# Optimization experiments

Measured on AMD Instinct MI355X. Metric: run time of the kernel, lower is better.

Reference implementation:

```python
import jax, jax.numpy as jnp
import numpy as np

B, S, H = 2, 2048, 2048
FFN = 1024
E = 8
TOP_K = 2


def setup_inputs() -> dict:
    key = jax.random.key(0)
    ks = jax.random.split(key, 5)
    scale = 0.02
    hidden_states = jax.random.normal(ks[0], (B, S, H), dtype=jnp.float32)
    Wg = jax.random.normal(ks[1], (E, H), dtype=jnp.float32) * scale   # gate: Linear(H, E) weight
    W1 = jax.random.normal(ks[2], (E, FFN, H), dtype=jnp.float32) * scale  # stacked w1 per expert
    W3 = jax.random.normal(ks[3], (E, FFN, H), dtype=jnp.float32) * scale  # stacked w3 per expert
    W2 = jax.random.normal(ks[4], (E, H, FFN), dtype=jnp.float32) * scale  # stacked w2 per expert
    bias = jnp.zeros((E,), dtype=jnp.float32)  # e_score_correction_bias buffer
    return {"hidden_states": hidden_states, "Wg": Wg, "W1": W1, "W2": W2, "W3": W3, "bias": bias}


def reference(hidden_states, Wg, W1, W2, W3, bias):
    bsz, seq_len, hidden_dim = hidden_states.shape
    x = hidden_states.reshape(-1, hidden_dim)                 # [T, H]
    router_logits = x @ Wg.T                                  # [T, E]
    routing_weights = jax.nn.sigmoid(router_logits.astype(jnp.float32))
    scores = routing_weights + bias                           # bias only affects selection
    _, top_k_index = jax.lax.top_k(scores, TOP_K)             # [T, K]
    top_k_weights = jnp.take_along_axis(routing_weights, top_k_index, axis=1)
    top_k_weights = top_k_weights / top_k_weights.sum(axis=-1, keepdims=True)
    top_k_weights = top_k_weights.astype(x.dtype)
    # per-token per-expert combine weight (0 for non-selected experts)
    one_hot = jax.nn.one_hot(top_k_index, Wg.shape[0], dtype=x.dtype)  # [T, K, E]
    expert_w = jnp.einsum('tk,tke->te', top_k_weights, one_hot)        # [T, E]
    # SwiGLU expert MLPs applied via stacked (grouped) GEMMs
    h1 = jnp.einsum('th,efh->tef', x, W1)                     # [T, E, FFN]
    h3 = jnp.einsum('th,efh->tef', x, W3)
    g = jax.nn.silu(h1) * h3 * expert_w[:, :, None]           # scale before down-proj
    out = jnp.einsum('tef,ehf->th', g, W2)                    # weighted combine
    return out.reshape(bsz, seq_len, hidden_dim)
```

## Files before the change

### kernel.cpp

```cpp
#include <hip/hip_runtime.h>
#include <hip/hip_bf16.h>


#define T_TOK 4096
#define H_DIM 2048
#define FFN_D 1024
#define NE    8

typedef __attribute__((ext_vector_type(8))) short          bf16x8;
typedef __attribute__((ext_vector_type(4))) float          f32x4;
typedef __attribute__((ext_vector_type(4))) unsigned short us4;

#define N4_PER_W ((size_t)NE * FFN_D * H_DIM / 4)
#define RB_ROUTER 1024u
#define CB_CONV   8192u

__device__ __forceinline__ unsigned short f2bf(float f) {
  unsigned u = __builtin_bit_cast(unsigned, f);
  u += 0x7fffu + ((u >> 16) & 1u);
  return (unsigned short)(u >> 16);
}
__device__ __forceinline__ float bf2f(unsigned short u) {
  return __builtin_bit_cast(float, ((unsigned)u) << 16);
}
__device__ __forceinline__ void async16(const void* g, void* l) {
  __builtin_amdgcn_global_load_lds((const __attribute__((address_space(1))) void*)g,
                                   (__attribute__((address_space(3))) void*)l, 16, 0, 0);
}

__global__ void router_conv_kernel(const float* __restrict__ x,
                                   const float* __restrict__ Wg,
                                   const float* __restrict__ bias,
                                   unsigned* __restrict__ epair,
                                   float* __restrict__ wpair,
                                   unsigned short* __restrict__ Xb,
                                   const float* __restrict__ W1, unsigned short* __restrict__ W1b,
                                   const float* __restrict__ W3, unsigned short* __restrict__ W3b) {
  if (blockIdx.x >= RB_ROUTER) {
    size_t b0 = (size_t)(blockIdx.x - RB_ROUTER) * 1024;
#pragma unroll
    for (int k = 0; k < 4; k++) {
      size_t i = b0 + k * 256 + threadIdx.x;
      const float* s; unsigned short* d;
      if (i < N4_PER_W) { s = W1; d = W1b; } else { s = W3; d = W3b; i -= N4_PER_W; }
      float4 v = ((const float4*)s)[i];
      us4 o; o.x = f2bf(v.x); o.y = f2bf(v.y); o.z = f2bf(v.z); o.w = f2bf(v.w);
      ((us4*)d)[i] = o;
    }
    return;
  }
  const int wv   = threadIdx.x >> 6;
  const int lane = threadIdx.x & 63;
  const int t    = blockIdx.x * 4 + wv;

  const float4* xr = (const float4*)(x + (size_t)t * H_DIM);
  us4*          xb = (us4*)(Xb + (size_t)t * H_DIM);

  float acc[NE];
#pragma unroll
  for (int e = 0; e < NE; e++) acc[e] = 0.f;

#pragma unroll
  for (int j = 0; j < 8; j++) {
    int i4 = j * 64 + lane;
    float4 v = xr[i4];
    us4 d; d.x = f2bf(v.x); d.y = f2bf(v.y); d.z = f2bf(v.z); d.w = f2bf(v.w);
    xb[i4] = d;
#pragma unroll
    for (int e = 0; e < NE; e++) {
      float4 w = ((const float4*)(Wg + e * H_DIM))[i4];
      acc[e] += v.x * w.x + v.y * w.y + v.z * w.z + v.w * w.w;
    }
  }
#pragma unroll
  for (int e = 0; e < NE; e++) {
#pragma unroll
    for (int m = 32; m >= 1; m >>= 1) acc[e] += __shfl_xor(acc[e], m, 64);
  }

  if (lane == 0) {
    float sig[NE], sc[NE];
#pragma unroll
    for (int e = 0; e < NE; e++) {
      sig[e] = 1.f / (1.f + expf(-acc[e]));
      sc[e]  = sig[e] + bias[e];
    }
    int i1 = 0; float v1 = sc[0];
#pragma unroll
    for (int e = 1; e < NE; e++) if (sc[e] > v1) { v1 = sc[e]; i1 = e; }
    int i2 = -1; float v2 = -1e30f;
#pragma unroll
    for (int e = 0; e < NE; e++) if (e != i1 && sc[e] > v2) { v2 = sc[e]; i2 = e; }
    float w1 = sig[i1], w2 = sig[i2];
    float s = w1 + w2;
    epair[t] = (unsigned)i1 | ((unsigned)i2 << 8);
    wpair[2 * t]     = w1 / s;
    wpair[2 * t + 1] = w2 / s;
  }
}

__global__ void compact_kernel(const unsigned* __restrict__ epair,
                               const float* __restrict__ wpair,
                               int* __restrict__ cnt,
                               int* __restrict__ base,
                               int* __restrict__ rows,
                               float* __restrict__ wts,
                               int* __restrict__ t2s) {
  const int e    = threadIdx.x >> 6;
  const int lane = threadIdx.x & 63;
  const unsigned long long ltmask = ((unsigned long long)1 << lane) - 1;
  __shared__ int cnts[NE];

  int count = 0;
  for (int c = 0; c < T_TOK; c += 64) {
    int t = c + lane;
    unsigned ep = epair[t];
    bool m1 = ((ep & 255u) == (unsigned)e);
    bool m2 = (((ep >> 8) & 255u) == (unsigned)e);
    unsigned long long b1 = __ballot(m1);
    if (m1) {
      int p = count + __popcll(b1 & ltmask);
      rows[e * T_TOK + p] = t;
      wts [e * T_TOK + p] = wpair[2 * t];
      t2s[2 * t] = (e << 12) | p;
    }
    count += __popcll(b1);
    unsigned long long b2 = __ballot(m2);
    if (m2) {
      int p = count + __popcll(b2 & ltmask);
      rows[e * T_TOK + p] = t;
      wts [e * T_TOK + p] = wpair[2 * t + 1];
      t2s[2 * t + 1] = (e << 12) | p;
    }
    count += __popcll(b2);
  }
  if (lane == 0) { cnts[e] = count; cnt[e] = count; }
  __syncthreads();
  if (threadIdx.x == 0) {
    int s = 0;
    for (int i = 0; i < NE; i++) { base[i] = s; s += cnts[i]; }
    base[NE] = s;
  }
}

__launch_bounds__(256)
__global__ void upproj_fast(const unsigned short* __restrict__ Xb,
                            const unsigned short* __restrict__ W1b,
                            const unsigned short* __restrict__ W3b,
                            const int* __restrict__ cnt,
                            const int* __restrict__ base,
                            const int* __restrict__ rows,
                            const float* __restrict__ wts,
                            unsigned short* __restrict__ G,
                            const float* __restrict__ W2, unsigned short* __restrict__ W2b) {
  if (blockIdx.z == NE) {
    size_t flat = (size_t)blockIdx.y * 16 + blockIdx.x;
    size_t b0 = flat * 8192;
#pragma unroll
    for (int k = 0; k < 32; k++) {
      size_t i = b0 + (size_t)k * 256 + threadIdx.x;
      float4 v = ((const float4*)W2)[i];
      us4 o; o.x = f2bf(v.x); o.y = f2bf(v.y); o.z = f2bf(v.z); o.w = f2bf(v.w);
      ((us4*)W2b)[i] = o;
    }
    return;
  }
  const int e  = blockIdx.z;
  const int m0 = blockIdx.y * 128;
  const int n0 = blockIdx.x * 64;
  const int ce = cnt[e];
  if (m0 >= ce) return;

  __shared__ __align__(16) unsigned short As [128 * 32];
  __shared__ __align__(16) unsigned short B1s[64 * 32];
  __shared__ __align__(16) unsigned short B3s[64 * 32];
  __shared__ int   t_ids[128];
  __shared__ float w_lds[128];

  const int tid = threadIdx.x;
  if (tid < 128) {
    int i = m0 + tid;
    if (i < ce) { t_ids[tid] = rows[e * T_TOK + i]; w_lds[tid] = wts[e * T_TOK + i]; }
    else        { t_ids[tid] = 0;                   w_lds[tid] = 0.f; }
  }
  __syncthreads();

  const int lane = tid & 63;
  const int wv   = tid >> 6;

  const unsigned short* gA[2];
#pragma unroll
  for (int c = 0; c < 2; c++) {
    int r = wv * 32 + c * 16 + (lane >> 2);
    gA[c] = Xb + (size_t)t_ids[r] * H_DIM + (lane & 3) * 8;
  }
  const size_t wrow = (size_t)(n0 + wv * 16 + (lane >> 2));
  const unsigned short* gB1 = W1b + (size_t)e * FFN_D * H_DIM + wrow * H_DIM + (lane & 3) * 8;
  const unsigned short* gB3 = W3b + (size_t)e * FFN_D * H_DIM + wrow * H_DIM + (lane & 3) * 8;
  unsigned short* lA0 = &As [(wv * 32 + 0)  * 32];
  unsigned short* lA1 = &As [(wv * 32 + 16) * 32];
  unsigned short* lB1 = &B1s[(wv * 16) * 32];
  unsigned short* lB3 = &B3s[(wv * 16) * 32];

  const int wm = (wv & 1) * 64;
  const int wn = (wv >> 1) * 32;
  const int qk = (lane >> 4) * 8;
  const int lr = lane & 15;

  f32x4 acc1[4][2], acc3[4][2];
#pragma unroll
  for (int mi = 0; mi < 4; mi++)
#pragma unroll
    for (int ni = 0; ni < 2; ni++) { acc1[mi][ni] = (f32x4)0.f; acc3[mi][ni] = (f32x4)0.f; }

  for (int kt = 0; kt < H_DIM; kt += 32) {
    async16(gA[0] + kt, lA0);
    async16(gA[1] + kt, lA1);
    async16(gB1 + kt,   lB1);
    async16(gB3 + kt,   lB3);
    __syncthreads();

    bf16x8 a[4], b1[2], b3[2];
#pragma unroll
    for (int mi = 0; mi < 4; mi++)
      a[mi] = *(const bf16x8*)&As[(wm + mi * 16 + lr) * 32 + qk];
#pragma unroll
    for (int ni = 0; ni < 2; ni++) {
      b1[ni] = *(const bf16x8*)&B1s[(wn + ni * 16 + lr) * 32 + qk];
      b3[ni] = *(const bf16x8*)&B3s[(wn + ni * 16 + lr) * 32 + qk];
    }
#pragma unroll
    for (int mi = 0; mi < 4; mi++)
#pragma unroll
      for (int ni = 0; ni < 2; ni++) {
        acc1[mi][ni] = __builtin_amdgcn_mfma_f32_16x16x32_bf16(a[mi], b1[ni], acc1[mi][ni], 0, 0, 0);
        acc3[mi][ni] = __builtin_amdgcn_mfma_f32_16x16x32_bf16(a[mi], b3[ni], acc3[mi][ni], 0, 0, 0);
      }
    __syncthreads();
  }

  const int be = base[e];
#pragma unroll
  for (int mi = 0; mi < 4; mi++)
#pragma unroll
    for (int ni = 0; ni < 2; ni++)
#pragma unroll
      for (int r = 0; r < 4; r++) {
        int row = wm + mi * 16 + (lane >> 4) * 4 + r;
        int col = wn + ni * 16 + lr;
        int i = m0 + row;
        if (i < ce) {
          float h1 = acc1[mi][ni][r];
          float h3 = acc3[mi][ni][r];
          float g  = h1 / (1.f + expf(-h1)) * h3 * w_lds[row];
          G[(size_t)(be + i) * FFN_D + n0 + col] = f2bf(g);
        }
      }
}

__launch_bounds__(256)
__global__ void downproj_fast(const unsigned short* __restrict__ G,
                              const unsigned short* __restrict__ W2b,
                              const int* __restrict__ cnt,
                              const int* __restrict__ base,
                              unsigned short* __restrict__ Gd) {
  const int e  = blockIdx.z;
  const int m0 = blockIdx.y * 128;
  const int n0 = blockIdx.x * 128;
  const int ce = cnt[e];
  if (m0 >= ce) return;
  const int be = base[e];

  __shared__ __align__(16) unsigned short As[128 * 32];
  __shared__ __align__(16) unsigned short Bs[128 * 32];

  const int tid  = threadIdx.x;
  const int lane = tid & 63;
  const int wv   = tid >> 6;

  const unsigned short* gA[2];
  const unsigned short* gB[2];
#pragma unroll
  for (int c = 0; c < 2; c++) {
    int r = m0 + wv * 32 + c * 16 + (lane >> 2);
    if (r >= ce) r = ce - 1;
    gA[c] = G + (size_t)(be + r) * FFN_D + (lane & 3) * 8;
    int rb = wv * 32 + c * 16 + (lane >> 2);
    gB[c] = W2b + (size_t)e * H_DIM * FFN_D + (size_t)(n0 + rb) * FFN_D + (lane & 3) * 8;
  }
  unsigned short* lA[2] = { &As[(wv * 32 + 0) * 32], &As[(wv * 32 + 16) * 32] };
  unsigned short* lB[2] = { &Bs[(wv * 32 + 0) * 32], &Bs[(wv * 32 + 16) * 32] };

  const int wm = (wv & 1) * 64;
  const int wn = (wv >> 1) * 64;
  const int qk = (lane >> 4) * 8;
  const int lr = lane & 15;

  f32x4 acc[4][4];
#pragma unroll
  for (int mi = 0; mi < 4; mi++)
#pragma unroll
    for (int ni = 0; ni < 4; ni++) acc[mi][ni] = (f32x4)0.f;

  for (int kt = 0; kt < FFN_D; kt += 32) {
    async16(gA[0] + kt, lA[0]);
    async16(gA[1] + kt, lA[1]);
    async16(gB[0] + kt, lB[0]);
    async16(gB[1] + kt, lB[1]);
    __syncthreads();

    bf16x8 a[4], b[4];
#pragma unroll
    for (int mi = 0; mi < 4; mi++)
      a[mi] = *(const bf16x8*)&As[(wm + mi * 16 + lr) * 32 + qk];
#pragma unroll
    for (int ni = 0; ni < 4; ni++)
      b[ni] = *(const bf16x8*)&Bs[(wn + ni * 16 + lr) * 32 + qk];
#pragma unroll
    for (int mi = 0; mi < 4; mi++)
#pragma unroll
      for (int ni = 0; ni < 4; ni++)
        acc[mi][ni] = __builtin_amdgcn_mfma_f32_16x16x32_bf16(a[mi], b[ni], acc[mi][ni], 0, 0, 0);
    __syncthreads();
  }

#pragma unroll
  for (int mi = 0; mi < 4; mi++)
#pragma unroll
    for (int ni = 0; ni < 4; ni++)
#pragma unroll
      for (int r = 0; r < 4; r++) {
        int row = wm + mi * 16 + (lane >> 4) * 4 + r;
        int col = wn + ni * 16 + lr;
        int i = m0 + row;
        if (i < ce)
          Gd[(size_t)(be + i) * H_DIM + n0 + col] = f2bf(acc[mi][ni][r]);
      }
}

__global__ void combine_kernel(const unsigned short* __restrict__ Gd,
                               const int* __restrict__ base,
                               const int* __restrict__ tok2slot,
                               float* __restrict__ out) {
  const int t = blockIdx.x;
  const int v1 = tok2slot[2 * t], v2 = tok2slot[2 * t + 1];
  const int s1 = base[v1 >> 12] + (v1 & 4095);
  const int s2 = base[v2 >> 12] + (v2 & 4095);
  const us4* r1 = (const us4*)(Gd + (size_t)s1 * H_DIM);
  const us4* r2 = (const us4*)(Gd + (size_t)s2 * H_DIM);
  float4* o = (float4*)(out + (size_t)t * H_DIM);
#pragma unroll
  for (int j = 0; j < 2; j++) {
    int i = j * 256 + threadIdx.x;
    us4 a = r1[i], b = r2[i];
    float4 r;
    r.x = bf2f(a.x) + bf2f(b.x);
    r.y = bf2f(a.y) + bf2f(b.y);
    r.z = bf2f(a.z) + bf2f(b.z);
    r.w = bf2f(a.w) + bf2f(b.w);
    o[i] = r;
  }
}

extern "C" void kernel_launch(void* const* d_in, const int* in_sizes, int n_in,
                              void* d_out, int out_size, void* d_ws, size_t ws_size,
                              hipStream_t stream) {
  (void)in_sizes; (void)n_in; (void)out_size; (void)ws_size;
  const float* x    = (const float*)d_in[0];
  const float* Wg   = (const float*)d_in[1];
  const float* W1   = (const float*)d_in[2];
  const float* W2   = (const float*)d_in[3];
  const float* W3   = (const float*)d_in[4];
  const float* bias = (const float*)d_in[5];
  float* out = (float*)d_out;

  char* ws = (char*)d_ws;
  const size_t OFF_CNT   = 0;
  const size_t OFF_BASE  = 64;
  const size_t OFF_T2S   = 1024;
  const size_t OFF_ROWS  = 65536;
  const size_t OFF_WTS   = OFF_ROWS + 131072;
  const size_t OFF_EPAIR = OFF_WTS + 131072;
  const size_t OFF_WPAIR = OFF_EPAIR + 16384;
  const size_t OFF_XB    = 1048576;
  const size_t OFF_W1B   = OFF_XB + 16777216;
  const size_t OFF_W3B   = OFF_W1B + 33554432;
  const size_t OFF_G     = OFF_W3B + 33554432;
  const size_t OFF_W2B   = OFF_G + 16777216;

  int*   cnt   = (int*)(ws + OFF_CNT);
  int*   base  = (int*)(ws + OFF_BASE);
  int*   t2s   = (int*)(ws + OFF_T2S);
  int*   rows  = (int*)(ws + OFF_ROWS);
  float* wts   = (float*)(ws + OFF_WTS);
  unsigned* epair = (unsigned*)(ws + OFF_EPAIR);
  float* wpair = (float*)(ws + OFF_WPAIR);
  unsigned short* Xb  = (unsigned short*)(ws + OFF_XB);
  unsigned short* W1b = (unsigned short*)(ws + OFF_W1B);
  unsigned short* W3b = (unsigned short*)(ws + OFF_W3B);
  unsigned short* W2b = (unsigned short*)(ws + OFF_W2B);
  unsigned short* Gd  = (unsigned short*)(ws + OFF_W1B);
  unsigned short* G   = (unsigned short*)(ws + OFF_G);

  router_conv_kernel<<<RB_ROUTER + CB_CONV, 256, 0, stream>>>(
      x, Wg, bias, epair, wpair, Xb, W1, W1b, W3, W3b);

  compact_kernel<<<1, 512, 0, stream>>>(epair, wpair, cnt, base, rows, wts, t2s);

  dim3 g2(FFN_D / 64, T_TOK / 128, NE + 1);
  upproj_fast<<<g2, 256, 0, stream>>>(Xb, W1b, W3b, cnt, base, rows, wts, G, W2, W2b);

  dim3 g3(H_DIM / 128, T_TOK / 128, NE);
  downproj_fast<<<g3, 256, 0, stream>>>(G, W2b, cnt, base, Gd);

  combine_kernel<<<T_TOK, 256, 0, stream>>>(Gd, base, t2s, out);
}
```

Measured before the change: 442.5 us.

## Fuse fp32-to-bf16 weight conversion into grouped GEMM tile loads

Removes the separate passes that convert W1, W3 and W2 from fp32 to bf16 in workspace. The up- and down-projection kernels now read fp32 weights straight from global memory into registers, round them to bf16 and write them into LDS, prefetching the next K-tile's weights one iteration ahead. This saves a full read and write of every weight matrix and one launch's worth of blocks. In exchange, each weight tile is now fetched as fp32 (twice the bytes) every time an M-block uses it, and the B operand moves from async global-to-LDS loads to register-staged stores.

```diff
diff --git a/kernel.cpp b/kernel.cpp
--- a/kernel.cpp
+++ b/kernel.cpp
@@ -10,10 +10,9 @@
 typedef __attribute__((ext_vector_type(8))) short          bf16x8;
 typedef __attribute__((ext_vector_type(4))) float          f32x4;
 typedef __attribute__((ext_vector_type(4))) unsigned short us4;
-
-#define N4_PER_W ((size_t)NE * FFN_D * H_DIM / 4)
+typedef __attribute__((ext_vector_type(8))) unsigned short us8;
+
 #define RB_ROUTER 1024u
-#define CB_CONV   8192u
 
 __device__ __forceinline__ unsigned short f2bf(float f) {
   unsigned u = __builtin_bit_cast(unsigned, f);
@@ -23,32 +22,23 @@
 __device__ __forceinline__ float bf2f(unsigned short u) {
   return __builtin_bit_cast(float, ((unsigned)u) << 16);
 }
+__device__ __forceinline__ us8 f8bf(float4 a, float4 b) {
+  us8 o;
+  o[0] = f2bf(a.x); o[1] = f2bf(a.y); o[2] = f2bf(a.z); o[3] = f2bf(a.w);
+  o[4] = f2bf(b.x); o[5] = f2bf(b.y); o[6] = f2bf(b.z); o[7] = f2bf(b.w);
+  return o;
+}
 __device__ __forceinline__ void async16(const void* g, void* l) {
   __builtin_amdgcn_global_load_lds((const __attribute__((address_space(1))) void*)g,
                                    (__attribute__((address_space(3))) void*)l, 16, 0, 0);
 }
 
-__global__ void router_conv_kernel(const float* __restrict__ x,
-                                   const float* __restrict__ Wg,
-                                   const float* __restrict__ bias,
-                                   unsigned* __restrict__ epair,
-                                   float* __restrict__ wpair,
-                                   unsigned short* __restrict__ Xb,
-                                   const float* __restrict__ W1, unsigned short* __restrict__ W1b,
-                                   const float* __restrict__ W3, unsigned short* __restrict__ W3b) {
-  if (blockIdx.x >= RB_ROUTER) {
-    size_t b0 = (size_t)(blockIdx.x - RB_ROUTER) * 1024;
-#pragma unroll
-    for (int k = 0; k < 4; k++) {
-      size_t i = b0 + k * 256 + threadIdx.x;
-      const float* s; unsigned short* d;
-      if (i < N4_PER_W) { s = W1; d = W1b; } else { s = W3; d = W3b; i -= N4_PER_W; }
-      float4 v = ((const float4*)s)[i];
-      us4 o; o.x = f2bf(v.x); o.y = f2bf(v.y); o.z = f2bf(v.z); o.w = f2bf(v.w);
-      ((us4*)d)[i] = o;
-    }
-    return;
-  }
+__global__ void router_kernel(const float* __restrict__ x,
+                              const float* __restrict__ Wg,
+                              const float* __restrict__ bias,
+                              unsigned* __restrict__ epair,
+                              float* __restrict__ wpair,
+                              unsigned short* __restrict__ Xb) {
   const int wv   = threadIdx.x >> 6;
   const int lane = threadIdx.x & 63;
   const int t    = blockIdx.x * 4 + wv;
@@ -145,26 +135,13 @@
 
 __launch_bounds__(256)
 __global__ void upproj_fast(const unsigned short* __restrict__ Xb,
-                            const unsigned short* __restrict__ W1b,
-                            const unsigned short* __restrict__ W3b,
+                            const float* __restrict__ W1,
+                            const float* __restrict__ W3,
                             const int* __restrict__ cnt,
                             const int* __restrict__ base,
                             const int* __restrict__ rows,
                             const float* __restrict__ wts,
-                            unsigned short* __restrict__ G,
-                            const float* __restrict__ W2, unsigned short* __restrict__ W2b) {
-  if (blockIdx.z == NE) {
-    size_t flat = (size_t)blockIdx.y * 16 + blockIdx.x;
-    size_t b0 = flat * 8192;
-#pragma unroll
-    for (int k = 0; k < 32; k++) {
-      size_t i = b0 + (size_t)k * 256 + threadIdx.x;
-      float4 v = ((const float4*)W2)[i];
-      us4 o; o.x = f2bf(v.x); o.y = f2bf(v.y); o.z = f2bf(v.z); o.w = f2bf(v.w);
-      ((us4*)W2b)[i] = o;
-    }
-    return;
-  }
+                            unsigned short* __restrict__ G) {
   const int e  = blockIdx.z;
   const int m0 = blockIdx.y * 128;
   const int n0 = blockIdx.x * 64;
@@ -194,13 +171,13 @@
     int r = wv * 32 + c * 16 + (lane >> 2);
     gA[c] = Xb + (size_t)t_ids[r] * H_DIM + (lane & 3) * 8;
   }
-  const size_t wrow = (size_t)(n0 + wv * 16 + (lane >> 2));
-  const unsigned short* gB1 = W1b + (size_t)e * FFN_D * H_DIM + wrow * H_DIM + (lane & 3) * 8;
-  const unsigned short* gB3 = W3b + (size_t)e * FFN_D * H_DIM + wrow * H_DIM + (lane & 3) * 8;
-  unsigned short* lA0 = &As [(wv * 32 + 0)  * 32];
-  unsigned short* lA1 = &As [(wv * 32 + 16) * 32];
-  unsigned short* lB1 = &B1s[(wv * 16) * 32];
-  unsigned short* lB3 = &B3s[(wv * 16) * 32];
+  unsigned short* lA0 = &As[(wv * 32 + 0)  * 32];
+  unsigned short* lA1 = &As[(wv * 32 + 16) * 32];
+
+  const int brow = n0 + wv * 16 + (lane >> 2);
+  const float* gB1 = W1 + (size_t)e * FFN_D * H_DIM + (size_t)brow * H_DIM + (lane & 3) * 8;
+  const float* gB3 = W3 + (size_t)e * FFN_D * H_DIM + (size_t)brow * H_DIM + (lane & 3) * 8;
+  const int bidx = (wv * 16 + (lane >> 2)) * 32 + (lane & 3) * 8;
 
   const int wm = (wv & 1) * 64;
   const int wn = (wv >> 1) * 32;
@@ -213,11 +190,24 @@
 #pragma unroll
     for (int ni = 0; ni < 2; ni++) { acc1[mi][ni] = (f32x4)0.f; acc3[mi][ni] = (f32x4)0.f; }
 
+  float4 p0 = *(const float4*)(gB1 + 0);
+  float4 p1 = *(const float4*)(gB1 + 4);
+  float4 p2 = *(const float4*)(gB3 + 0);
+  float4 p3 = *(const float4*)(gB3 + 4);
+
   for (int kt = 0; kt < H_DIM; kt += 32) {
     async16(gA[0] + kt, lA0);
     async16(gA[1] + kt, lA1);
-    async16(gB1 + kt,   lB1);
-    async16(gB3 + kt,   lB3);
+
+    float4 c0 = p0, c1 = p1, c2 = p2, c3 = p3;
+    int ktn = (kt + 32 < H_DIM) ? kt + 32 : kt;
+    p0 = *(const float4*)(gB1 + ktn);
+    p1 = *(const float4*)(gB1 + ktn + 4);
+    p2 = *(const float4*)(gB3 + ktn);
+    p3 = *(const float4*)(gB3 + ktn + 4);
+
+    *(us8*)&B1s[bidx] = f8bf(c0, c1);
+    *(us8*)&B3s[bidx] = f8bf(c2, c3);
     __syncthreads();
 
     bf16x8 a[4], b1[2], b3[2];
@@ -260,7 +250,7 @@
 
 __launch_bounds__(256)
 __global__ void downproj_fast(const unsigned short* __restrict__ G,
-                              const unsigned short* __restrict__ W2b,
+                              const float* __restrict__ W2,
                               const int* __restrict__ cnt,
                               const int* __restrict__ base,
                               unsigned short* __restrict__ Gd) {
@@ -279,17 +269,20 @@
   const int wv   = tid >> 6;
 
   const unsigned short* gA[2];
-  const unsigned short* gB[2];
 #pragma unroll
   for (int c = 0; c < 2; c++) {
     int r = m0 + wv * 32 + c * 16 + (lane >> 2);
     if (r >= ce) r = ce - 1;
     gA[c] = G + (size_t)(be + r) * FFN_D + (lane & 3) * 8;
-    int rb = wv * 32 + c * 16 + (lane >> 2);
-    gB[c] = W2b + (size_t)e * H_DIM * FFN_D + (size_t)(n0 + rb) * FFN_D + (lane & 3) * 8;
   }
   unsigned short* lA[2] = { &As[(wv * 32 + 0) * 32], &As[(wv * 32 + 16) * 32] };
-  unsigned short* lB[2] = { &Bs[(wv * 32 + 0) * 32], &Bs[(wv * 32 + 16) * 32] };
+
+  const int rb0 = wv * 32 + (lane >> 2);
+  const int rb1 = rb0 + 16;
+  const float* gB0 = W2 + (size_t)e * H_DIM * FFN_D + (size_t)(n0 + rb0) * FFN_D + (lane & 3) * 8;
+  const float* gB1 = W2 + (size_t)e * H_DIM * FFN_D + (size_t)(n0 + rb1) * FFN_D + (lane & 3) * 8;
+  const int bi0 = rb0 * 32 + (lane & 3) * 8;
+  const int bi1 = rb1 * 32 + (lane & 3) * 8;
 
   const int wm = (wv & 1) * 64;
   const int wn = (wv >> 1) * 64;
@@ -302,11 +295,24 @@
 #pragma unroll
     for (int ni = 0; ni < 4; ni++) acc[mi][ni] = (f32x4)0.f;
 
+  float4 p0 = *(const float4*)(gB0 + 0);
+  float4 p1 = *(const float4*)(gB0 + 4);
+  float4 p2 = *(const float4*)(gB1 + 0);
+  float4 p3 = *(const float4*)(gB1 + 4);
+
   for (int kt = 0; kt < FFN_D; kt += 32) {
     async16(gA[0] + kt, lA[0]);
     async16(gA[1] + kt, lA[1]);
-    async16(gB[0] + kt, lB[0]);
-    async16(gB[1] + kt, lB[1]);
+
+    float4 c0 = p0, c1 = p1, c2 = p2, c3 = p3;
+    int ktn = (kt + 32 < FFN_D) ? kt + 32 : kt;
+    p0 = *(const float4*)(gB0 + ktn);
+    p1 = *(const float4*)(gB0 + ktn + 4);
+    p2 = *(const float4*)(gB1 + ktn);
+    p3 = *(const float4*)(gB1 + ktn + 4);
+
+    *(us8*)&Bs[bi0] = f8bf(c0, c1);
+    *(us8*)&Bs[bi1] = f8bf(c2, c3);
     __syncthreads();
 
     bf16x8 a[4], b[4];
@@ -383,10 +389,8 @@
   const size_t OFF_EPAIR = OFF_WTS + 131072;
   const size_t OFF_WPAIR = OFF_EPAIR + 16384;
   const size_t OFF_XB    = 1048576;
-  const size_t OFF_W1B   = OFF_XB + 16777216;
-  const size_t OFF_W3B   = OFF_W1B + 33554432;
-  const size_t OFF_G     = OFF_W3B + 33554432;
-  const size_t OFF_W2B   = OFF_G + 16777216;
+  const size_t OFF_G     = OFF_XB + 16777216;
+  const size_t OFF_GD    = OFF_G + 16777216;
 
   int*   cnt   = (int*)(ws + OFF_CNT);
   int*   base  = (int*)(ws + OFF_BASE);
@@ -396,22 +400,18 @@
   unsigned* epair = (unsigned*)(ws + OFF_EPAIR);
   float* wpair = (float*)(ws + OFF_WPAIR);
   unsigned short* Xb  = (unsigned short*)(ws + OFF_XB);
-  unsigned short* W1b = (unsigned short*)(ws + OFF_W1B);
-  unsigned short* W3b = (unsigned short*)(ws + OFF_W3B);
-  unsigned short* W2b = (unsigned short*)(ws + OFF_W2B);
-  unsigned short* Gd  = (unsigned short*)(ws + OFF_W1B);
   unsigned short* G   = (unsigned short*)(ws + OFF_G);
-
-  router_conv_kernel<<<RB_ROUTER + CB_CONV, 256, 0, stream>>>(
-      x, Wg, bias, epair, wpair, Xb, W1, W1b, W3, W3b);
+  unsigned short* Gd  = (unsigned short*)(ws + OFF_GD);
+
+  router_kernel<<<RB_ROUTER, 256, 0, stream>>>(x, Wg, bias, epair, wpair, Xb);
 
   compact_kernel<<<1, 512, 0, stream>>>(epair, wpair, cnt, base, rows, wts, t2s);
 
-  dim3 g2(FFN_D / 64, T_TOK / 128, NE + 1);
-  upproj_fast<<<g2, 256, 0, stream>>>(Xb, W1b, W3b, cnt, base, rows, wts, G, W2, W2b);
+  dim3 g2(FFN_D / 64, T_TOK / 128, NE);
+  upproj_fast<<<g2, 256, 0, stream>>>(Xb, W1, W3, cnt, base, rows, wts, G);
 
   dim3 g3(H_DIM / 128, T_TOK / 128, NE);
-  downproj_fast<<<g3, 256, 0, stream>>>(G, W2b, cnt, base, Gd);
+  downproj_fast<<<g3, 256, 0, stream>>>(G, W2, cnt, base, Gd);
 
   combine_kernel<<<T_TOK, 256, 0, stream>>>(Gd, base, t2s, out);
 }
```

Result: slower. 559.7 us (+26.5%).

## Triple-buffer grouped GEMM LDS loads with swizzle and packed bf16 conversion

Applied to the files above, without the earlier changes.

Both expert GEMM kernels now use a three-stage LDS ring. Global-to-LDS async loads for tile k+2 are issued before computing tile k, and a vmcnt wait plus a single barrier per iteration replaces the two full syncthreads, so memory latency can overlap with MFMA work. A column XOR swizzle is applied to both the global source column and the LDS read offset to reduce bank conflicts. The fp32-to-bf16 conversions switch to the packed v_cvt_pk_bf16_f32 instruction. The cost is triple the LDS footprint, which may lower occupancy, and the pipeline now relies on correct manual vmcnt accounting.

```diff
diff --git a/kernel.cpp b/kernel.cpp
--- a/kernel.cpp
+++ b/kernel.cpp
@@ -22,6 +22,12 @@
 }
 __device__ __forceinline__ float bf2f(unsigned short u) {
   return __builtin_bit_cast(float, ((unsigned)u) << 16);
+}
+__device__ __forceinline__ us4 f4bf(float4 v) {
+  union { us4 o; unsigned u[2]; } r;
+  asm("v_cvt_pk_bf16_f32 %0, %1, %2" : "=v"(r.u[0]) : "v"(v.x), "v"(v.y));
+  asm("v_cvt_pk_bf16_f32 %0, %1, %2" : "=v"(r.u[1]) : "v"(v.z), "v"(v.w));
+  return r.o;
 }
 __device__ __forceinline__ void async16(const void* g, void* l) {
   __builtin_amdgcn_global_load_lds((const __attribute__((address_space(1))) void*)g,
@@ -44,8 +50,7 @@
       const float* s; unsigned short* d;
       if (i < N4_PER_W) { s = W1; d = W1b; } else { s = W3; d = W3b; i -= N4_PER_W; }
       float4 v = ((const float4*)s)[i];
-      us4 o; o.x = f2bf(v.x); o.y = f2bf(v.y); o.z = f2bf(v.z); o.w = f2bf(v.w);
-      ((us4*)d)[i] = o;
+      ((us4*)d)[i] = f4bf(v);
     }
     return;
   }
@@ -64,8 +69,7 @@
   for (int j = 0; j < 8; j++) {
     int i4 = j * 64 + lane;
     float4 v = xr[i4];
-    us4 d; d.x = f2bf(v.x); d.y = f2bf(v.y); d.z = f2bf(v.z); d.w = f2bf(v.w);
-    xb[i4] = d;
+    xb[i4] = f4bf(v);
 #pragma unroll
     for (int e = 0; e < NE; e++) {
       float4 w = ((const float4*)(Wg + e * H_DIM))[i4];
@@ -160,8 +164,7 @@
     for (int k = 0; k < 32; k++) {
       size_t i = b0 + (size_t)k * 256 + threadIdx.x;
       float4 v = ((const float4*)W2)[i];
-      us4 o; o.x = f2bf(v.x); o.y = f2bf(v.y); o.z = f2bf(v.z); o.w = f2bf(v.w);
-      ((us4*)W2b)[i] = o;
+      ((us4*)W2b)[i] = f4bf(v);
     }
     return;
   }
@@ -171,9 +174,9 @@
   const int ce = cnt[e];
   if (m0 >= ce) return;
 
-  __shared__ __align__(16) unsigned short As [128 * 32];
-  __shared__ __align__(16) unsigned short B1s[64 * 32];
-  __shared__ __align__(16) unsigned short B3s[64 * 32];
+  __shared__ __align__(16) unsigned short As [3][128 * 32];
+  __shared__ __align__(16) unsigned short B1s[3][64 * 32];
+  __shared__ __align__(16) unsigned short B3s[3][64 * 32];
   __shared__ int   t_ids[128];
   __shared__ float w_lds[128];
 
@@ -188,23 +191,26 @@
   const int lane = tid & 63;
   const int wv   = tid >> 6;
 
+  const int sA   = (lane >> 3) & 3;
+  const int gcol = ((lane & 3) ^ sA) * 8;
+  const int rxor = ((lane & 15) >> 1) & 3;
+  const int qx   = ((lane >> 4) ^ rxor) * 8;
+
   const unsigned short* gA[2];
 #pragma unroll
   for (int c = 0; c < 2; c++) {
     int r = wv * 32 + c * 16 + (lane >> 2);
-    gA[c] = Xb + (size_t)t_ids[r] * H_DIM + (lane & 3) * 8;
+    gA[c] = Xb + (size_t)t_ids[r] * H_DIM + gcol;
   }
   const size_t wrow = (size_t)(n0 + wv * 16 + (lane >> 2));
-  const unsigned short* gB1 = W1b + (size_t)e * FFN_D * H_DIM + wrow * H_DIM + (lane & 3) * 8;
-  const unsigned short* gB3 = W3b + (size_t)e * FFN_D * H_DIM + wrow * H_DIM + (lane & 3) * 8;
-  unsigned short* lA0 = &As [(wv * 32 + 0)  * 32];
-  unsigned short* lA1 = &As [(wv * 32 + 16) * 32];
-  unsigned short* lB1 = &B1s[(wv * 16) * 32];
-  unsigned short* lB3 = &B3s[(wv * 16) * 32];
+  const unsigned short* gB1 = W1b + (size_t)e * FFN_D * H_DIM + wrow * H_DIM + gcol;
+  const unsigned short* gB3 = W3b + (size_t)e * FFN_D * H_DIM + wrow * H_DIM + gcol;
+  const int dA0 = (wv * 32 + 0)  * 32;
+  const int dA1 = (wv * 32 + 16) * 32;
+  const int dB  = (wv * 16) * 32;
 
   const int wm = (wv & 1) * 64;
   const int wn = (wv >> 1) * 32;
-  const int qk = (lane >> 4) * 8;
   const int lr = lane & 15;
 
   f32x4 acc1[4][2], acc3[4][2];
@@ -213,21 +219,33 @@
 #pragma unroll
     for (int ni = 0; ni < 2; ni++) { acc1[mi][ni] = (f32x4)0.f; acc3[mi][ni] = (f32x4)0.f; }
 
-  for (int kt = 0; kt < H_DIM; kt += 32) {
-    async16(gA[0] + kt, lA0);
-    async16(gA[1] + kt, lA1);
-    async16(gB1 + kt,   lB1);
-    async16(gB3 + kt,   lB3);
-    __syncthreads();
+#define STAGE_UP(KT, BUF)                          \
+  do {                                             \
+    async16(gA[0] + (KT), &As [BUF][dA0]);         \
+    async16(gA[1] + (KT), &As [BUF][dA1]);         \
+    async16(gB1  + (KT), &B1s[BUF][dB]);           \
+    async16(gB3  + (KT), &B3s[BUF][dB]);           \
+  } while (0)
+
+  STAGE_UP(0, 0);
+  STAGE_UP(32, 1);
+  asm volatile("s_waitcnt vmcnt(4)" ::: "memory");
+  __builtin_amdgcn_s_barrier();
+
+  for (int k = 0; k < H_DIM / 32; ++k) {
+    const int kt2 = (k + 2) * 32;
+    const int cb  = k % 3;
+    if (kt2 < H_DIM) STAGE_UP(kt2, (k + 2) % 3);
+    __builtin_amdgcn_sched_barrier(0);
 
     bf16x8 a[4], b1[2], b3[2];
 #pragma unroll
     for (int mi = 0; mi < 4; mi++)
-      a[mi] = *(const bf16x8*)&As[(wm + mi * 16 + lr) * 32 + qk];
+      a[mi] = *(const bf16x8*)&As[cb][(wm + mi * 16 + lr) * 32 + qx];
 #pragma unroll
     for (int ni = 0; ni < 2; ni++) {
-      b1[ni] = *(const bf16x8*)&B1s[(wn + ni * 16 + lr) * 32 + qk];
-      b3[ni] = *(const bf16x8*)&B3s[(wn + ni * 16 + lr) * 32 + qk];
+      b1[ni] = *(const bf16x8*)&B1s[cb][(wn + ni * 16 + lr) * 32 + qx];
+      b3[ni] = *(const bf16x8*)&B3s[cb][(wn + ni * 16 + lr) * 32 + qx];
     }
 #pragma unroll
     for (int mi = 0; mi < 4; mi++)
@@ -236,8 +254,14 @@
         acc1[mi][ni] = __builtin_amdgcn_mfma_f32_16x16x32_bf16(a[mi], b1[ni], acc1[mi][ni], 0, 0, 0);
         acc3[mi][ni] = __builtin_amdgcn_mfma_f32_16x16x32_bf16(a[mi], b3[ni], acc3[mi][ni], 0, 0, 0);
       }
-    __syncthreads();
-  }
+
+    if (kt2 < H_DIM) asm volatile("s_waitcnt vmcnt(4)" ::: "memory");
+    else             asm volatile("s_waitcnt vmcnt(0)" ::: "memory");
+    __builtin_amdgcn_sched_barrier(0);
+    __builtin_amdgcn_s_barrier();
+    __builtin_amdgcn_sched_barrier(0);
+  }
+#undef STAGE_UP
 
   const int be = base[e];
 #pragma unroll
@@ -271,29 +295,33 @@
   if (m0 >= ce) return;
   const int be = base[e];
 
-  __shared__ __align__(16) unsigned short As[128 * 32];
-  __shared__ __align__(16) unsigned short Bs[128 * 32];
+  __shared__ __align__(16) unsigned short As[3][128 * 32];
+  __shared__ __align__(16) unsigned short Bs[3][128 * 32];
 
   const int tid  = threadIdx.x;
   const int lane = tid & 63;
   const int wv   = tid >> 6;
 
+  const int sA   = (lane >> 3) & 3;
+  const int gcol = ((lane & 3) ^ sA) * 8;
+  const int rxor = ((lane & 15) >> 1) & 3;
+  const int qx   = ((lane >> 4) ^ rxor) * 8;
+
   const unsigned short* gA[2];
   const unsigned short* gB[2];
 #pragma unroll
   for (int c = 0; c < 2; c++) {
     int r = m0 + wv * 32 + c * 16 + (lane >> 2);
     if (r >= ce) r = ce - 1;
-    gA[c] = G + (size_t)(be + r) * FFN_D + (lane & 3) * 8;
+    gA[c] = G + (size_t)(be + r) * FFN_D + gcol;
     int rb = wv * 32 + c * 16 + (lane >> 2);
-    gB[c] = W2b + (size_t)e * H_DIM * FFN_D + (size_t)(n0 + rb) * FFN_D + (lane & 3) * 8;
-  }
-  unsigned short* lA[2] = { &As[(wv * 32 + 0) * 32], &As[(wv * 32 + 16) * 32] };
-  unsigned short* lB[2] = { &Bs[(wv * 32 + 0) * 32], &Bs[(wv * 32 + 16) * 32] };
+    gB[c] = W2b + (size_t)e * H_DIM * FFN_D + (size_t)(n0 + rb) * FFN_D + gcol;
+  }
+  const int dA0 = (wv * 32 + 0)  * 32;
+  const int dA1 = (wv * 32 + 16) * 32;
 
   const int wm = (wv & 1) * 64;
   const int wn = (wv >> 1) * 64;
-  const int qk = (lane >> 4) * 8;
   const int lr = lane & 15;
 
   f32x4 acc[4][4];
@@ -302,27 +330,45 @@
 #pragma unroll
     for (int ni = 0; ni < 4; ni++) acc[mi][ni] = (f32x4)0.f;
 
-  for (int kt = 0; kt < FFN_D; kt += 32) {
-    async16(gA[0] + kt, lA[0]);
-    async16(gA[1] + kt, lA[1]);
-    async16(gB[0] + kt, lB[0]);
-    async16(gB[1] + kt, lB[1]);
-    __syncthreads();
+#define STAGE_DN(KT, BUF)                          \
+  do {                                             \
+    async16(gA[0] + (KT), &As[BUF][dA0]);          \
+    async16(gA[1] + (KT), &As[BUF][dA1]);          \
+    async16(gB[0] + (KT), &Bs[BUF][dA0]);          \
+    async16(gB[1] + (KT), &Bs[BUF][dA1]);          \
+  } while (0)
+
+  STAGE_DN(0, 0);
+  STAGE_DN(32, 1);
+  asm volatile("s_waitcnt vmcnt(4)" ::: "memory");
+  __builtin_amdgcn_s_barrier();
+
+  for (int k = 0; k < FFN_D / 32; ++k) {
+    const int kt2 = (k + 2) * 32;
+    const int cb  = k % 3;
+    if (kt2 < FFN_D) STAGE_DN(kt2, (k + 2) % 3);
+    __builtin_amdgcn_sched_barrier(0);
 
     bf16x8 a[4], b[4];
 #pragma unroll
     for (int mi = 0; mi < 4; mi++)
-      a[mi] = *(const bf16x8*)&As[(wm + mi * 16 + lr) * 32 + qk];
+      a[mi] = *(const bf16x8*)&As[cb][(wm + mi * 16 + lr) * 32 + qx];
 #pragma unroll
     for (int ni = 0; ni < 4; ni++)
-      b[ni] = *(const bf16x8*)&Bs[(wn + ni * 16 + lr) * 32 + qk];
+      b[ni] = *(const bf16x8*)&Bs[cb][(wn + ni * 16 + lr) * 32 + qx];
 #pragma unroll
     for (int mi = 0; mi < 4; mi++)
 #pragma unroll
       for (int ni = 0; ni < 4; ni++)
         acc[mi][ni] = __builtin_amdgcn_mfma_f32_16x16x32_bf16(a[mi], b[ni], acc[mi][ni], 0, 0, 0);
-    __syncthreads();
-  }
+
+    if (kt2 < FFN_D) asm volatile("s_waitcnt vmcnt(4)" ::: "memory");
+    else             asm volatile("s_waitcnt vmcnt(0)" ::: "memory");
+    __builtin_amdgcn_sched_barrier(0);
+    __builtin_amdgcn_s_barrier();
+    __builtin_amdgcn_sched_barrier(0);
+  }
+#undef STAGE_DN
 
 #pragma unroll
   for (int mi = 0; mi < 4; mi++)
```

Result: slower. 453.3 us (+2.5%).
